# Optimization experiments

Measured on AMD Instinct MI355X. Metric: run time of the kernel, lower is better.

Reference implementation:

```python
import jax, jax.numpy as jnp
import numpy as np

ALPHA = 1.702
LIMIT = 7.0
EPS = 1e-5
TOP_K = 4


def setup_inputs() -> dict:
    key = jax.random.key(0)
    ks = jax.random.split(key, 8)
    B, S, H, I, E = 2, 512, 2048, 2048, 16
    return {
        "x": jax.random.normal(ks[0], (B, S, H), jnp.float32),
        "norm_w": jnp.ones((H,), jnp.float32),
        "gate_w": jax.random.normal(ks[1], (E, H), jnp.float32) * 0.02,
        "gate_b": jax.random.normal(ks[2], (E,), jnp.float32) * 0.02,
        "w1": jax.random.normal(ks[3], (E, 2 * I, H), jnp.float32) * 0.02,
        "b1": jax.random.normal(ks[4], (E, 2 * I), jnp.float32) * 0.02,
        "w2": jax.random.normal(ks[5], (E, H, I), jnp.float32) * 0.02,
        "b2": jax.random.normal(ks[6], (E, H), jnp.float32) * 0.02,
    }


def reference(x, norm_w, gate_w, gate_b, w1, b1, w2, b2):
    B, S, H = x.shape
    M = B * S
    E = gate_w.shape[0]
    xf = x.reshape(M, H)
    # RMSNorm
    t = xf * jax.lax.rsqrt(jnp.mean(xf * xf, axis=-1, keepdims=True) + EPS) * norm_w
    # Router: top-k over logits, then softmax over the selected k (sm_first=False)
    logits = t @ gate_w.T + gate_b  # [M, E]
    vals, idx = jax.lax.top_k(logits, TOP_K)
    gates_k = jax.nn.softmax(vals, axis=-1)  # [M, k]
    # Scatter top-k gate weights into dense [M, E] combine matrix
    G = jnp.zeros((M, E), x.dtype).at[jnp.arange(M)[:, None], idx].set(gates_k)
    # Expert MLP1 (all experts, combined sparsely below): [E, M, 2I]
    h = jnp.einsum('mh,eoh->emo', t, w1) + b1[:, None, :]
    # SwiGLU with clamp (gpt-oss): interleaved gate/linear columns
    a = jnp.minimum(h[..., ::2], LIMIT)
    b = jnp.clip(h[..., 1::2], -LIMIT, LIMIT)
    act = a * jax.nn.sigmoid(ALPHA * a) * (b + 1.0)  # [E, M, I]
    # Expert MLP2: [E, M, H]
    y = jnp.einsum('emi,edi->emd', act, w2) + b2[:, None, :]
    # Combine with gate weights (gammas scale full per-expert output incl. bias)
    delta = jnp.einsum('me,emd->md', G, y)
    return x + delta.reshape(B, S, H)
```

## Files before the change

kernel.cpp:

```cpp
#include <hip/hip_runtime.h>
#include <hip/hip_bf16.h>

constexpr int MTOK = 1024;
constexpr int HDIM = 2048;
constexpr int IDIM = 2048;
constexpr int NEXP = 16;
constexpr int TOPK = 4;
constexpr int NA   = MTOK * TOPK;

#define ALPHA_C 1.702f
#define LIMIT_C 7.0f
#define RMS_EPS 1e-5f

using short8 = __attribute__((ext_vector_type(8))) short;
using f32x4  = __attribute__((ext_vector_type(4))) float;

__device__ __forceinline__ unsigned short f2bf(float f) {
    unsigned u = __builtin_bit_cast(unsigned, f);
    u += 0x7fffu + ((u >> 16) & 1u);
    return (unsigned short)(u >> 16);
}

__device__ __forceinline__ unsigned pack2bf(float lo, float hi) {
    return (unsigned)f2bf(lo) | ((unsigned)f2bf(hi) << 16);
}

__device__ __forceinline__ short8 cvt8(const float4 a, const float4 b) {
    union { short8 s; unsigned u[4]; } r;
    r.u[0] = pack2bf(a.x, a.y);
    r.u[1] = pack2bf(a.z, a.w);
    r.u[2] = pack2bf(b.x, b.y);
    r.u[3] = pack2bf(b.z, b.w);
    return r.s;
}

__global__ __launch_bounds__(256) void k_router(
    const float* __restrict__ x, const float* __restrict__ norm_w,
    const float* __restrict__ gate_w, const float* __restrict__ gate_b,
    unsigned short* __restrict__ t_bf,
    int* __restrict__ counts, int* __restrict__ idx_of,
    int* __restrict__ slot_of, float* __restrict__ gate_mk)
{
    __shared__ float t_lds[HDIM];
    __shared__ float red[4];
    __shared__ float logits[NEXP];

    const int m   = blockIdx.x;
    const int tid = threadIdx.x;
    const float* xr = x + (size_t)m * HDIM;

    float4 v0 = ((const float4*)xr)[tid * 2];
    float4 v1 = ((const float4*)xr)[tid * 2 + 1];
    float ss = v0.x*v0.x + v0.y*v0.y + v0.z*v0.z + v0.w*v0.w
             + v1.x*v1.x + v1.y*v1.y + v1.z*v1.z + v1.w*v1.w;
    #pragma unroll
    for (int off = 32; off > 0; off >>= 1) ss += __shfl_down(ss, off);
    if ((tid & 63) == 0) red[tid >> 6] = ss;
    __syncthreads();
    float tot = red[0] + red[1] + red[2] + red[3];
    float scale = rsqrtf(tot / (float)HDIM + RMS_EPS);

    float4 n0 = ((const float4*)norm_w)[tid * 2];
    float4 n1 = ((const float4*)norm_w)[tid * 2 + 1];
    float t[8];
    t[0]=v0.x*scale*n0.x; t[1]=v0.y*scale*n0.y; t[2]=v0.z*scale*n0.z; t[3]=v0.w*scale*n0.w;
    t[4]=v1.x*scale*n1.x; t[5]=v1.y*scale*n1.y; t[6]=v1.z*scale*n1.z; t[7]=v1.w*scale*n1.w;
    short8 pk;
    #pragma unroll
    for (int j = 0; j < 8; ++j) {
        t_lds[tid * 8 + j] = t[j];
        pk[j] = (short)f2bf(t[j]);
    }
    *(short8*)(t_bf + (size_t)m * HDIM + tid * 8) = pk;
    __syncthreads();

    const int e = tid >> 4, j = tid & 15;
    const float4* gw4 = (const float4*)(gate_w + (size_t)e * HDIM);
    const float4* tl4 = (const float4*)t_lds;
    float part = 0.f;
    for (int h4 = j; h4 < HDIM / 4; h4 += 16) {
        float4 g = gw4[h4], tv = tl4[h4];
        part += g.x*tv.x + g.y*tv.y + g.z*tv.z + g.w*tv.w;
    }
    #pragma unroll
    for (int off = 8; off > 0; off >>= 1) part += __shfl_xor(part, off);
    if (j == 0) logits[e] = part + gate_b[e];
    __syncthreads();

    if (tid == 0) {
        float lv[NEXP];
        #pragma unroll
        for (int q = 0; q < NEXP; ++q) lv[q] = logits[q];
        int   sel[TOPK];
        float sv[TOPK];
        #pragma unroll
        for (int k = 0; k < TOPK; ++k) {
            float best = -1e30f; int bi = 0;
            for (int q = 0; q < NEXP; ++q)
                if (lv[q] > best) { best = lv[q]; bi = q; }
            sel[k] = bi; sv[k] = best; lv[bi] = -1e30f;
        }
        float mx = sv[0], s = 0.f, g[TOPK];
        #pragma unroll
        for (int k = 0; k < TOPK; ++k) { g[k] = __expf(sv[k] - mx); s += g[k]; }
        float inv = 1.f / s;
        #pragma unroll
        for (int k = 0; k < TOPK; ++k) {
            int a = m * TOPK + k;
            int slot = atomicAdd(&counts[sel[k]], 1);
            idx_of[a]  = sel[k];
            slot_of[a] = slot;
            gate_mk[a] = g[k] * inv;
        }
    }
}

__global__ void k_remap(const int* __restrict__ idx_of, const int* __restrict__ slot_of,
                        const int* __restrict__ counts,
                        int* __restrict__ token_of, int* __restrict__ rowidx)
{
    int a = blockIdx.x * blockDim.x + threadIdx.x;
    if (a >= NA) return;
    int e = idx_of[a];
    int off = 0;
    for (int q = 0; q < NEXP; ++q) off += (q < e) ? counts[q] : 0;
    int r = off + slot_of[a];
    token_of[r] = a >> 2;
    rowidx[a]   = r;
}

__global__ __launch_bounds__(256, 2) void k_gemm1(
    const unsigned short* __restrict__ t_bf,
    const float* __restrict__ w1, const float* __restrict__ b1,
    const int* __restrict__ counts, const int* __restrict__ token_of,
    unsigned short* __restrict__ act)
{
    __shared__ unsigned char lB[2][5120];

    const int e = blockIdx.z;
    int ne = 0, roff = 0;
    #pragma unroll
    for (int q = 0; q < NEXP; ++q) {
        int cq = counts[q];
        roff += (q < e) ? cq : 0;
        ne    = (q == e) ? cq : ne;
    }
    const int brow = blockIdx.y * 320;
    if (brow >= ne) return;
    const int i0 = blockIdx.x * 32;
    const int tid = threadIdx.x;

    const int wv = tid >> 6, ln = tid & 63;
    const int lr = ln & 15, lk = ln >> 4;
    const int br = tid >> 2, bp = tid & 3;

    const unsigned short* aptr[5];
    #pragma unroll
    for (int mf = 0; mf < 5; ++mf) {
        int rg = brow + wv * 80 + mf * 16 + lr;
        int tok = token_of[roff + (rg < ne ? rg : 0)];
        aptr[mf] = t_bf + (size_t)tok * HDIM + lk * 8;
    }
    const int o = (br < 32) ? (2 * (i0 + br)) : (2 * (i0 + br - 32) + 1);
    const float* bsrc = w1 + ((size_t)e * (2 * IDIM) + o) * HDIM + bp * 8;

    short8 aE[5], aO[5];
    float4 bS0[2], bS1[2], bS2[2], bS3[2];
    f32x4  acc[5][4] = {};

    constexpr int NT = 64;

    #pragma unroll
    for (int mf = 0; mf < 5; ++mf) aE[mf] = *(const short8*)(aptr[mf]);
    {
        float4 p0 = *(const float4*)(bsrc);
        float4 p1 = *(const float4*)(bsrc + 4);
        *(short8*)(&lB[0][br * 80 + bp * 16]) = cvt8(p0, p1);
    }
    bS1[0] = *(const float4*)(bsrc + 32);  bS1[1] = *(const float4*)(bsrc + 36);
    bS2[0] = *(const float4*)(bsrc + 64);  bS2[1] = *(const float4*)(bsrc + 68);
    asm volatile("s_waitcnt lgkmcnt(0)" ::: "memory");
    __builtin_amdgcn_s_barrier();

#define GSTEP(T_, AU, AP, SPUB, SISS)                                                    \
    {                                                                                    \
        const int t_ = (T_);                                                             \
        if (t_ + 1 < NT) {                                          \
            _Pragma("unroll")                                                            \
            for (int mf = 0; mf < 5; ++mf)                                               \
                AP[mf] = *(const short8*)(aptr[mf] + (t_ + 1) * 32);                     \
        }                                                                                \
        if (t_ + 3 < NT) {                                         \
            SISS[0] = *(const float4*)(bsrc + (t_ + 3) * 32);                            \
            SISS[1] = *(const float4*)(bsrc + (t_ + 3) * 32 + 4);                        \
        }                                                                                \
        __builtin_amdgcn_sched_barrier(0);                      \
        if (t_ + 1 < NT)                                          \
            *(short8*)(&lB[(t_ + 1) & 1][br * 80 + bp * 16]) = cvt8(SPUB[0], SPUB[1]);   \
        short8 bfr[4];                                            \
        _Pragma("unroll")                                                                \
        for (int n = 0; n < 4; ++n)                                                      \
            bfr[n] = *(const short8*)(&lB[t_ & 1][(n * 16 + lr) * 80 + lk * 16]);        \
        _Pragma("unroll")                                                                \
        for (int mf = 0; mf < 5; ++mf)                                                   \
            _Pragma("unroll")                                                            \
            for (int n = 0; n < 4; ++n)                                                  \
                acc[mf][n] = __builtin_amdgcn_mfma_f32_16x16x32_bf16(                    \
                    AU[mf], bfr[n], acc[mf][n], 0, 0, 0);                                \
        asm volatile("s_waitcnt lgkmcnt(0)" ::: "memory");                               \
        __builtin_amdgcn_s_barrier();                                                    \
    }

    for (int t4 = 0; t4 < NT / 4; ++t4) {
        const int tb = t4 * 4;
        GSTEP(tb + 0, aE, aO, bS1, bS3)
        GSTEP(tb + 1, aO, aE, bS2, bS0)
        GSTEP(tb + 2, aE, aO, bS3, bS1)
        GSTEP(tb + 3, aO, aE, bS0, bS2)
    }
#undef GSTEP

    #pragma unroll
    for (int n = 0; n < 2; ++n) {
        const int i = i0 + n * 16 + lr;
        const float ba = b1[(size_t)e * (2 * IDIM) + 2 * i];
        const float bb = b1[(size_t)e * (2 * IDIM) + 2 * i + 1];
        #pragma unroll
        for (int mf = 0; mf < 5; ++mf) {
            #pragma unroll
            for (int r = 0; r < 4; ++r) {
                const int rg = brow + wv * 80 + mf * 16 + lk * 4 + r;
                if (rg < ne) {
                    float ha = acc[mf][n][r] + ba;
                    float hb = acc[mf][n + 2][r] + bb;
                    float a = fminf(ha, LIMIT_C);
                    float b = fminf(fmaxf(hb, -LIMIT_C), LIMIT_C);
                    float s = 1.f / (1.f + __expf(-ALPHA_C * a));
                    act[(size_t)(roff + rg) * IDIM + i] = f2bf(a * s * (b + 1.f));
                }
            }
        }
    }
}

__global__ __launch_bounds__(256, 2) void k_gemm2(
    const unsigned short* __restrict__ act,
    const float* __restrict__ w2, const float* __restrict__ b2,
    const int* __restrict__ counts, const int* __restrict__ token_of,
    unsigned short* __restrict__ ybuf)
{
    __shared__ unsigned char lB[2][5120];

    const int e = blockIdx.z;
    int ne = 0, roff = 0;
    #pragma unroll
    for (int q = 0; q < NEXP; ++q) {
        int cq = counts[q];
        roff += (q < e) ? cq : 0;
        ne    = (q == e) ? cq : ne;
    }
    const int brow = blockIdx.y * 320;
    if (brow >= ne) return;
    const int d0 = blockIdx.x * 64;
    const int tid = threadIdx.x;

    const int wv = tid >> 6, ln = tid & 63;
    const int lr = ln & 15, lk = ln >> 4;
    const int br = tid >> 2, bp = tid & 3;

    const unsigned short* aptr[5];
    #pragma unroll
    for (int mf = 0; mf < 5; ++mf) {
        int rg = brow + wv * 80 + mf * 16 + lr;
        int rc = (rg < ne) ? rg : 0;
        aptr[mf] = act + (size_t)(roff + rc) * IDIM + lk * 8;
    }
    const float* bsrc = w2 + ((size_t)e * HDIM + d0 + br) * IDIM + bp * 8;

    short8 aE[5], aO[5];
    float4 bS0[2], bS1[2], bS2[2], bS3[2];
    f32x4  acc[5][4] = {};

    constexpr int NT = 64;

    #pragma unroll
    for (int mf = 0; mf < 5; ++mf) aE[mf] = *(const short8*)(aptr[mf]);
    {
        float4 p0 = *(const float4*)(bsrc);
        float4 p1 = *(const float4*)(bsrc + 4);
        *(short8*)(&lB[0][br * 80 + bp * 16]) = cvt8(p0, p1);
    }
    bS1[0] = *(const float4*)(bsrc + 32);  bS1[1] = *(const float4*)(bsrc + 36);
    bS2[0] = *(const float4*)(bsrc + 64);  bS2[1] = *(const float4*)(bsrc + 68);
    asm volatile("s_waitcnt lgkmcnt(0)" ::: "memory");
    __builtin_amdgcn_s_barrier();

#define GSTEP(T_, AU, AP, SPUB, SISS)                                                    \
    {                                                                                    \
        const int t_ = (T_);                                                             \
        if (t_ + 1 < NT) {                                                               \
            _Pragma("unroll")                                                            \
            for (int mf = 0; mf < 5; ++mf)                                               \
                AP[mf] = *(const short8*)(aptr[mf] + (t_ + 1) * 32);                     \
        }                                                                                \
        if (t_ + 3 < NT) {                                                               \
            SISS[0] = *(const float4*)(bsrc + (t_ + 3) * 32);                            \
            SISS[1] = *(const float4*)(bsrc + (t_ + 3) * 32 + 4);                        \
        }                                                                                \
        __builtin_amdgcn_sched_barrier(0);                                               \
        if (t_ + 1 < NT)                                                                 \
            *(short8*)(&lB[(t_ + 1) & 1][br * 80 + bp * 16]) = cvt8(SPUB[0], SPUB[1]);   \
        short8 bfr[4];                                                                   \
        _Pragma("unroll")                                                                \
        for (int n = 0; n < 4; ++n)                                                      \
            bfr[n] = *(const short8*)(&lB[t_ & 1][(n * 16 + lr) * 80 + lk * 16]);        \
        _Pragma("unroll")                                                                \
        for (int mf = 0; mf < 5; ++mf)                                                   \
            _Pragma("unroll")                                                            \
            for (int n = 0; n < 4; ++n)                                                  \
                acc[mf][n] = __builtin_amdgcn_mfma_f32_16x16x32_bf16(                    \
                    AU[mf], bfr[n], acc[mf][n], 0, 0, 0);                                \
        asm volatile("s_waitcnt lgkmcnt(0)" ::: "memory");                               \
        __builtin_amdgcn_s_barrier();                                                    \
    }

    for (int t4 = 0; t4 < NT / 4; ++t4) {
        const int tb = t4 * 4;
        GSTEP(tb + 0, aE, aO, bS1, bS3)
        GSTEP(tb + 1, aO, aE, bS2, bS0)
        GSTEP(tb + 2, aE, aO, bS3, bS1)
        GSTEP(tb + 3, aO, aE, bS0, bS2)
    }
#undef GSTEP

    #pragma unroll
    for (int mf = 0; mf < 5; ++mf) {
        #pragma unroll
        for (int r = 0; r < 4; ++r) {
            const int rg = brow + wv * 80 + mf * 16 + lk * 4 + r;
            if (rg >= ne) continue;
            unsigned short* yrow = ybuf + (size_t)(roff + rg) * HDIM;
            #pragma unroll
            for (int n = 0; n < 4; ++n) {
                const int d = d0 + n * 16 + lr;
                yrow[d] = f2bf(acc[mf][n][r] + b2[(size_t)e * HDIM + d]);
            }
        }
    }
}

__global__ __launch_bounds__(256) void k_comb(
    const float* __restrict__ x, const unsigned short* __restrict__ ybuf,
    const int* __restrict__ rowidx, const float* __restrict__ gate_mk,
    float* __restrict__ out)
{
    __shared__ int   rws[TOPK];
    __shared__ float gws[TOPK];
    const int m = blockIdx.x;
    const int tid = threadIdx.x;
    if (tid < TOPK) {
        rws[tid] = rowidx[m * TOPK + tid];
        gws[tid] = gate_mk[m * TOPK + tid];
    }
    __syncthreads();
    const int d = tid * 8;
    float4 o0 = ((const float4*)(x + (size_t)m * HDIM + d))[0];
    float4 o1 = ((const float4*)(x + (size_t)m * HDIM + d))[1];
    #pragma unroll
    for (int k = 0; k < TOPK; ++k) {
        const float g = gws[k];
        short8 y = *(const short8*)(ybuf + (size_t)rws[k] * HDIM + d);
        float yv[8];
        #pragma unroll
        for (int j = 0; j < 8; ++j) {
            unsigned u = ((unsigned)(unsigned short)y[j]) << 16;
            yv[j] = __builtin_bit_cast(float, u);
        }
        o0.x += g * yv[0]; o0.y += g * yv[1]; o0.z += g * yv[2]; o0.w += g * yv[3];
        o1.x += g * yv[4]; o1.y += g * yv[5]; o1.z += g * yv[6]; o1.w += g * yv[7];
    }
    ((float4*)(out + (size_t)m * HDIM + d))[0] = o0;
    ((float4*)(out + (size_t)m * HDIM + d))[1] = o1;
}

extern "C" void kernel_launch(void* const* d_in, const int* in_sizes, int n_in,
                              void* d_out, int out_size, void* d_ws, size_t ws_size,
                              hipStream_t stream) {
    const float* x      = (const float*)d_in[0];
    const float* norm_w = (const float*)d_in[1];
    const float* gate_w = (const float*)d_in[2];
    const float* gate_b = (const float*)d_in[3];
    const float* w1     = (const float*)d_in[4];
    const float* b1     = (const float*)d_in[5];
    const float* w2     = (const float*)d_in[6];
    const float* b2     = (const float*)d_in[7];
    float* out = (float*)d_out;

    char* ws = (char*)d_ws;
    size_t off = 0;
    unsigned short* t_bf = (unsigned short*)(ws + off); off += (size_t)MTOK * HDIM * 2;
    unsigned short* actb = (unsigned short*)(ws + off); off += (size_t)NA * IDIM * 2;
    unsigned short* ybuf = (unsigned short*)(ws + off); off += (size_t)NA * HDIM * 2;
    int*   counts   = (int*)(ws + off);   off += 256;
    int*   idx_of   = (int*)(ws + off);   off += (size_t)NA * 4;
    int*   slot_of  = (int*)(ws + off);   off += (size_t)NA * 4;
    float* gate_mk  = (float*)(ws + off); off += (size_t)NA * 4;
    int*   token_of = (int*)(ws + off);   off += (size_t)NA * 4;
    int*   rowidx   = (int*)(ws + off);   off += (size_t)NA * 4;

    (void)hipMemsetAsync(counts, 0, 256, stream);
    k_router<<<MTOK, 256, 0, stream>>>(x, norm_w, gate_w, gate_b, t_bf,
                                       counts, idx_of, slot_of, gate_mk);
    k_remap<<<NA / 256, 256, 0, stream>>>(idx_of, slot_of, counts,
                                          token_of, rowidx);
    k_gemm1<<<dim3(IDIM / 32, (MTOK + 319) / 320, NEXP), 256, 0, stream>>>(
        t_bf, w1, b1, counts, token_of, actb);
    k_gemm2<<<dim3(HDIM / 64, (MTOK + 319) / 320, NEXP), 256, 0, stream>>>(
        actb, w2, b2, counts, token_of, ybuf);
    k_comb<<<MTOK, 256, 0, stream>>>(x, ybuf, rowidx, gate_mk, out);
}
```

Measured before the change: 410.9 us.

## Restructure expert GEMMs with wider tiles, direct-to-LDS fp32 weight loads, XCD-aware block mapping

Both expert GEMMs now use 512-thread blocks with 8 waves arranged 4x2, covering 320 rows by 256 weight columns per block instead of 320x64. Weight tiles are copied as fp32 straight into a triple-buffered LDS ring with global_load_lds, and converted to bf16 with v_cvt_pk_bf16_f32 when read for the MFMA. Blocks use a flat 1D grid decoded so that each XCD handles two experts, aiming to improve L2 reuse of weights. The goal is fewer register-staged global loads and more MFMA work per weight byte, at the cost of 96KB of LDS per block and reconverting each weight element once per wave that reads it.

```diff
diff --git a/kernel.cpp b/kernel.cpp
--- a/kernel.cpp
+++ b/kernel.cpp
@@ -21,17 +21,16 @@
     return (unsigned short)(u >> 16);
 }
 
-__device__ __forceinline__ unsigned pack2bf(float lo, float hi) {
-    return (unsigned)f2bf(lo) | ((unsigned)f2bf(hi) << 16);
-}
-
-__device__ __forceinline__ short8 cvt8(const float4 a, const float4 b) {
-    union { short8 s; unsigned u[4]; } r;
-    r.u[0] = pack2bf(a.x, a.y);
-    r.u[1] = pack2bf(a.z, a.w);
-    r.u[2] = pack2bf(b.x, b.y);
-    r.u[3] = pack2bf(b.z, b.w);
-    return r.s;
+__device__ __forceinline__ void gload16(const void* g, void* l) {
+    __builtin_amdgcn_global_load_lds(
+        (const __attribute__((address_space(1))) void*)g,
+        (__attribute__((address_space(3))) void*)l, 16, 0, 0);
+}
+
+__device__ __forceinline__ unsigned cvtpk(float lo, float hi) {
+    unsigned r;
+    asm volatile("v_cvt_pk_bf16_f32 %0, %1, %2" : "=v"(r) : "v"(lo), "v"(hi));
+    return r;
 }
 
 __global__ __launch_bounds__(256) void k_router(
@@ -129,15 +128,59 @@
     rowidx[a]   = r;
 }
 
-__global__ __launch_bounds__(256, 2) void k_gemm1(
+
+#define GEMM_STEP(T_, RB, WB, AU, AP, NTT)                                               \
+    {                                                                                    \
+        const int t_ = (T_);                                                             \
+        __builtin_amdgcn_s_barrier();                                                    \
+        const int tw = (t_ + 2 < (NTT)) ? (t_ + 2) : ((NTT) - 1);                        \
+        _Pragma("unroll")                                                                \
+        for (int j = 0; j < 4; ++j)                                                      \
+            gload16(bsrc + (size_t)j * BJSTR + (size_t)tw * 32,                          \
+                    lds + (WB) * 32768 + (wv * 4 + j) * 1024);                           \
+        const int ta = (t_ + 1 < (NTT)) ? (t_ + 1) : ((NTT) - 1);                        \
+        _Pragma("unroll")                                                                \
+        for (int mf = 0; mf < 5; ++mf)                                                   \
+            AP[mf] = *(const short8*)(aptr[mf] + ta * 32);                               \
+        asm volatile("s_waitcnt vmcnt(9)" ::: "memory");                                 \
+        __builtin_amdgcn_sched_barrier(0);                                               \
+        short8 bfr[8];                                                                   \
+        _Pragma("unroll")                                                                \
+        for (int n = 0; n < 8; ++n) {                                                    \
+            const int c_ = cfrag[n] + lr;                                                \
+            const unsigned char* cb = lds + (RB) * 32768 + (c_ >> 3) * 1024              \
+                                      + (c_ & 7) * 16 + lk * 256;                        \
+            f32x4 u0 = *(const f32x4*)(cb);                                              \
+            f32x4 u1 = *(const f32x4*)(cb + 128);                                        \
+            union { short8 s; unsigned u[4]; } r;                                        \
+            r.u[0] = cvtpk(u0[0], u0[1]); r.u[1] = cvtpk(u0[2], u0[3]);                  \
+            r.u[2] = cvtpk(u1[0], u1[1]); r.u[3] = cvtpk(u1[2], u1[3]);                  \
+            bfr[n] = r.s;                                                                \
+        }                                                                                \
+        _Pragma("unroll")                                                                \
+        for (int mf = 0; mf < 5; ++mf)                                                   \
+            _Pragma("unroll")                                                            \
+            for (int n = 0; n < 8; ++n)                                                  \
+                acc[mf][n] = __builtin_amdgcn_mfma_f32_16x16x32_bf16(                    \
+                    AU[mf], bfr[n], acc[mf][n], 0, 0, 0);                                \
+    }
+
+__global__ __launch_bounds__(512, 2) void k_gemm1(
     const unsigned short* __restrict__ t_bf,
     const float* __restrict__ w1, const float* __restrict__ b1,
     const int* __restrict__ counts, const int* __restrict__ token_of,
     unsigned short* __restrict__ act)
 {
-    __shared__ unsigned char lB[2][5120];
-
-    const int e = blockIdx.z;
+    __shared__ unsigned char lB[3 * 32768];
+
+    const int bid = blockIdx.x;
+    const int xcd = bid & 7;
+    const int jj  = bid >> 3;
+    const int e   = (xcd << 1) | (jj & 1);
+    const int rem = jj >> 1;
+    const int by  = rem >> 4;
+    const int bx  = rem & 15;
+
     int ne = 0, roff = 0;
     #pragma unroll
     for (int q = 0; q < NEXP; ++q) {
@@ -145,94 +188,75 @@
         roff += (q < e) ? cq : 0;
         ne    = (q == e) ? cq : ne;
     }
-    const int brow = blockIdx.y * 320;
+    const int brow = by * 320;
     if (brow >= ne) return;
-    const int i0 = blockIdx.x * 32;
+    const int i0 = bx * 128;
     const int tid = threadIdx.x;
 
     const int wv = tid >> 6, ln = tid & 63;
+    const int wm = wv >> 1, wn = wv & 1;
     const int lr = ln & 15, lk = ln >> 4;
-    const int br = tid >> 2, bp = tid & 3;
+
+    unsigned char* lds = lB;
+    constexpr int NT = 64;
 
     const unsigned short* aptr[5];
     #pragma unroll
     for (int mf = 0; mf < 5; ++mf) {
-        int rg = brow + wv * 80 + mf * 16 + lr;
+        int rg = brow + wm * 80 + mf * 16 + lr;
         int tok = token_of[roff + (rg < ne ? rg : 0)];
         aptr[mf] = t_bf + (size_t)tok * HDIM + lk * 8;
     }
-    const int o = (br < 32) ? (2 * (i0 + br)) : (2 * (i0 + br - 32) + 1);
-    const float* bsrc = w1 + ((size_t)e * (2 * IDIM) + o) * HDIM + bp * 8;
+
+    const int c7 = ln & 7, chunk = ln >> 3;
+    const int col0 = wv * 32 + c7;
+    const int o0 = (col0 < 128) ? (2 * (i0 + col0)) : (2 * (i0 + col0 - 128) + 1);
+    const float* bsrc = w1 + ((size_t)e * (2 * IDIM) + o0) * HDIM + chunk * 4;
+    const size_t BJSTR = (size_t)16 * HDIM;
+
+    int cfrag[8];
+    #pragma unroll
+    for (int n = 0; n < 4; ++n) { cfrag[n] = wn * 64 + n * 16; cfrag[n + 4] = 128 + wn * 64 + n * 16; }
 
     short8 aE[5], aO[5];
-    float4 bS0[2], bS1[2], bS2[2], bS3[2];
-    f32x4  acc[5][4] = {};
-
-    constexpr int NT = 64;
-
+    f32x4  acc[5][8] = {};
+
+    #pragma unroll
+    for (int j = 0; j < 4; ++j)
+        gload16(bsrc + (size_t)j * BJSTR, lds + (wv * 4 + j) * 1024);
     #pragma unroll
     for (int mf = 0; mf < 5; ++mf) aE[mf] = *(const short8*)(aptr[mf]);
-    {
-        float4 p0 = *(const float4*)(bsrc);
-        float4 p1 = *(const float4*)(bsrc + 4);
-        *(short8*)(&lB[0][br * 80 + bp * 16]) = cvt8(p0, p1);
-    }
-    bS1[0] = *(const float4*)(bsrc + 32);  bS1[1] = *(const float4*)(bsrc + 36);
-    bS2[0] = *(const float4*)(bsrc + 64);  bS2[1] = *(const float4*)(bsrc + 68);
-    asm volatile("s_waitcnt lgkmcnt(0)" ::: "memory");
-    __builtin_amdgcn_s_barrier();
-
-#define GSTEP(T_, AU, AP, SPUB, SISS)                                                    \
-    {                                                                                    \
-        const int t_ = (T_);                                                             \
-        if (t_ + 1 < NT) {                                          \
-            _Pragma("unroll")                                                            \
-            for (int mf = 0; mf < 5; ++mf)                                               \
-                AP[mf] = *(const short8*)(aptr[mf] + (t_ + 1) * 32);                     \
-        }                                                                                \
-        if (t_ + 3 < NT) {                                         \
-            SISS[0] = *(const float4*)(bsrc + (t_ + 3) * 32);                            \
-            SISS[1] = *(const float4*)(bsrc + (t_ + 3) * 32 + 4);                        \
-        }                                                                                \
-        __builtin_amdgcn_sched_barrier(0);                      \
-        if (t_ + 1 < NT)                                          \
-            *(short8*)(&lB[(t_ + 1) & 1][br * 80 + bp * 16]) = cvt8(SPUB[0], SPUB[1]);   \
-        short8 bfr[4];                                            \
-        _Pragma("unroll")                                                                \
-        for (int n = 0; n < 4; ++n)                                                      \
-            bfr[n] = *(const short8*)(&lB[t_ & 1][(n * 16 + lr) * 80 + lk * 16]);        \
-        _Pragma("unroll")                                                                \
-        for (int mf = 0; mf < 5; ++mf)                                                   \
-            _Pragma("unroll")                                                            \
-            for (int n = 0; n < 4; ++n)                                                  \
-                acc[mf][n] = __builtin_amdgcn_mfma_f32_16x16x32_bf16(                    \
-                    AU[mf], bfr[n], acc[mf][n], 0, 0, 0);                                \
-        asm volatile("s_waitcnt lgkmcnt(0)" ::: "memory");                               \
-        __builtin_amdgcn_s_barrier();                                                    \
-    }
-
-    for (int t4 = 0; t4 < NT / 4; ++t4) {
-        const int tb = t4 * 4;
-        GSTEP(tb + 0, aE, aO, bS1, bS3)
-        GSTEP(tb + 1, aO, aE, bS2, bS0)
-        GSTEP(tb + 2, aE, aO, bS3, bS1)
-        GSTEP(tb + 3, aO, aE, bS0, bS2)
-    }
-#undef GSTEP
-
-    #pragma unroll
-    for (int n = 0; n < 2; ++n) {
-        const int i = i0 + n * 16 + lr;
+    #pragma unroll
+    for (int j = 0; j < 4; ++j)
+        gload16(bsrc + (size_t)j * BJSTR + 32, lds + 32768 + (wv * 4 + j) * 1024);
+
+    for (int q = 0; q < 10; ++q) {
+        const int tb = q * 6;
+        GEMM_STEP(tb + 0, 0, 2, aE, aO, NT)
+        GEMM_STEP(tb + 1, 1, 0, aO, aE, NT)
+        GEMM_STEP(tb + 2, 2, 1, aE, aO, NT)
+        GEMM_STEP(tb + 3, 0, 2, aO, aE, NT)
+        GEMM_STEP(tb + 4, 1, 0, aE, aO, NT)
+        GEMM_STEP(tb + 5, 2, 1, aO, aE, NT)
+    }
+    GEMM_STEP(60, 0, 2, aE, aO, NT)
+    GEMM_STEP(61, 1, 0, aO, aE, NT)
+    GEMM_STEP(62, 2, 1, aE, aO, NT)
+    GEMM_STEP(63, 0, 2, aO, aE, NT)
+
+    #pragma unroll
+    for (int n = 0; n < 4; ++n) {
+        const int i = i0 + wn * 64 + n * 16 + lr;
         const float ba = b1[(size_t)e * (2 * IDIM) + 2 * i];
         const float bb = b1[(size_t)e * (2 * IDIM) + 2 * i + 1];
         #pragma unroll
         for (int mf = 0; mf < 5; ++mf) {
             #pragma unroll
             for (int r = 0; r < 4; ++r) {
-                const int rg = brow + wv * 80 + mf * 16 + lk * 4 + r;
+                const int rg = brow + wm * 80 + mf * 16 + lk * 4 + r;
                 if (rg < ne) {
                     float ha = acc[mf][n][r] + ba;
-                    float hb = acc[mf][n + 2][r] + bb;
+                    float hb = acc[mf][n + 4][r] + bb;
                     float a = fminf(ha, LIMIT_C);
                     float b = fminf(fmaxf(hb, -LIMIT_C), LIMIT_C);
                     float s = 1.f / (1.f + __expf(-ALPHA_C * a));
@@ -243,15 +267,22 @@
     }
 }
 
-__global__ __launch_bounds__(256, 2) void k_gemm2(
+__global__ __launch_bounds__(512, 2) void k_gemm2(
     const unsigned short* __restrict__ act,
     const float* __restrict__ w2, const float* __restrict__ b2,
     const int* __restrict__ counts, const int* __restrict__ token_of,
     unsigned short* __restrict__ ybuf)
 {
-    __shared__ unsigned char lB[2][5120];
-
-    const int e = blockIdx.z;
+    __shared__ unsigned char lB[3 * 32768];
+
+    const int bid = blockIdx.x;
+    const int xcd = bid & 7;
+    const int jj  = bid >> 3;
+    const int e   = (xcd << 1) | (jj & 1);
+    const int rem = jj >> 1;
+    const int by  = rem >> 3;
+    const int bx  = rem & 7;
+
     int ne = 0, roff = 0;
     #pragma unroll
     for (int q = 0; q < NEXP; ++q) {
@@ -259,90 +290,71 @@
         roff += (q < e) ? cq : 0;
         ne    = (q == e) ? cq : ne;
     }
-    const int brow = blockIdx.y * 320;
+    const int brow = by * 320;
     if (brow >= ne) return;
-    const int d0 = blockIdx.x * 64;
+    const int d0 = bx * 256;
     const int tid = threadIdx.x;
 
     const int wv = tid >> 6, ln = tid & 63;
+    const int wm = wv >> 1, wn = wv & 1;
     const int lr = ln & 15, lk = ln >> 4;
-    const int br = tid >> 2, bp = tid & 3;
+
+    unsigned char* lds = lB;
+    constexpr int NT = 64;
 
     const unsigned short* aptr[5];
     #pragma unroll
     for (int mf = 0; mf < 5; ++mf) {
-        int rg = brow + wv * 80 + mf * 16 + lr;
+        int rg = brow + wm * 80 + mf * 16 + lr;
         int rc = (rg < ne) ? rg : 0;
         aptr[mf] = act + (size_t)(roff + rc) * IDIM + lk * 8;
     }
-    const float* bsrc = w2 + ((size_t)e * HDIM + d0 + br) * IDIM + bp * 8;
+
+    const int c7 = ln & 7, chunk = ln >> 3;
+    const int col0 = wv * 32 + c7;
+    const float* bsrc = w2 + ((size_t)e * HDIM + d0 + col0) * IDIM + chunk * 4;
+    const size_t BJSTR = (size_t)8 * IDIM;
+
+    int cfrag[8];
+    #pragma unroll
+    for (int n = 0; n < 8; ++n) cfrag[n] = wn * 128 + n * 16;
 
     short8 aE[5], aO[5];
-    float4 bS0[2], bS1[2], bS2[2], bS3[2];
-    f32x4  acc[5][4] = {};
-
-    constexpr int NT = 64;
-
+    f32x4  acc[5][8] = {};
+
+    #pragma unroll
+    for (int j = 0; j < 4; ++j)
+        gload16(bsrc + (size_t)j * BJSTR, lds + (wv * 4 + j) * 1024);
     #pragma unroll
     for (int mf = 0; mf < 5; ++mf) aE[mf] = *(const short8*)(aptr[mf]);
-    {
-        float4 p0 = *(const float4*)(bsrc);
-        float4 p1 = *(const float4*)(bsrc + 4);
-        *(short8*)(&lB[0][br * 80 + bp * 16]) = cvt8(p0, p1);
-    }
-    bS1[0] = *(const float4*)(bsrc + 32);  bS1[1] = *(const float4*)(bsrc + 36);
-    bS2[0] = *(const float4*)(bsrc + 64);  bS2[1] = *(const float4*)(bsrc + 68);
-    asm volatile("s_waitcnt lgkmcnt(0)" ::: "memory");
-    __builtin_amdgcn_s_barrier();
-
-#define GSTEP(T_, AU, AP, SPUB, SISS)                                                    \
-    {                                                                                    \
-        const int t_ = (T_);                                                             \
-        if (t_ + 1 < NT) {                                                               \
-            _Pragma("unroll")                                                            \
-            for (int mf = 0; mf < 5; ++mf)                                               \
-                AP[mf] = *(const short8*)(aptr[mf] + (t_ + 1) * 32);                     \
-        }                                                                                \
-        if (t_ + 3 < NT) {                                                               \
-            SISS[0] = *(const float4*)(bsrc + (t_ + 3) * 32);                            \
-            SISS[1] = *(const float4*)(bsrc + (t_ + 3) * 32 + 4);                        \
-        }                                                                                \
-        __builtin_amdgcn_sched_barrier(0);                                               \
-        if (t_ + 1 < NT)                                                                 \
-            *(short8*)(&lB[(t_ + 1) & 1][br * 80 + bp * 16]) = cvt8(SPUB[0], SPUB[1]);   \
-        short8 bfr[4];                                                                   \
-        _Pragma("unroll")                                                                \
-        for (int n = 0; n < 4; ++n)                                                      \
-            bfr[n] = *(const short8*)(&lB[t_ & 1][(n * 16 + lr) * 80 + lk * 16]);        \
-        _Pragma("unroll")                                                                \
-        for (int mf = 0; mf < 5; ++mf)                                                   \
-            _Pragma("unroll")                                                            \
-            for (int n = 0; n < 4; ++n)                                                  \
-                acc[mf][n] = __builtin_amdgcn_mfma_f32_16x16x32_bf16(                    \
-                    AU[mf], bfr[n], acc[mf][n], 0, 0, 0);                                \
-        asm volatile("s_waitcnt lgkmcnt(0)" ::: "memory");                               \
-        __builtin_amdgcn_s_barrier();                                                    \
-    }
-
-    for (int t4 = 0; t4 < NT / 4; ++t4) {
-        const int tb = t4 * 4;
-        GSTEP(tb + 0, aE, aO, bS1, bS3)
-        GSTEP(tb + 1, aO, aE, bS2, bS0)
-        GSTEP(tb + 2, aE, aO, bS3, bS1)
-        GSTEP(tb + 3, aO, aE, bS0, bS2)
-    }
-#undef GSTEP
+    #pragma unroll
+    for (int j = 0; j < 4; ++j)
+        gload16(bsrc + (size_t)j * BJSTR + 32, lds + 32768 + (wv * 4 + j) * 1024);
+
+    for (int q = 0; q < 10; ++q) {
+        const int tb = q * 6;
+        GEMM_STEP(tb + 0, 0, 2, aE, aO, NT)
+        GEMM_STEP(tb + 1, 1, 0, aO, aE, NT)
+        GEMM_STEP(tb + 2, 2, 1, aE, aO, NT)
+        GEMM_STEP(tb + 3, 0, 2, aO, aE, NT)
+        GEMM_STEP(tb + 4, 1, 0, aE, aO, NT)
+        GEMM_STEP(tb + 5, 2, 1, aO, aE, NT)
+    }
+    GEMM_STEP(60, 0, 2, aE, aO, NT)
+    GEMM_STEP(61, 1, 0, aO, aE, NT)
+    GEMM_STEP(62, 2, 1, aE, aO, NT)
+    GEMM_STEP(63, 0, 2, aO, aE, NT)
 
     #pragma unroll
     for (int mf = 0; mf < 5; ++mf) {
         #pragma unroll
         for (int r = 0; r < 4; ++r) {
-            const int rg = brow + wv * 80 + mf * 16 + lk * 4 + r;
+            const int rg = brow + wm * 80 + mf * 16 + lk * 4 + r;
             if (rg >= ne) continue;
             unsigned short* yrow = ybuf + (size_t)(roff + rg) * HDIM;
             #pragma unroll
-            for (int n = 0; n < 4; ++n) {
-                const int d = d0 + n * 16 + lr;
+            for (int n = 0; n < 8; ++n) {
+                const int d = d0 + cfrag[n] + lr;
                 yrow[d] = f2bf(acc[mf][n][r] + b2[(size_t)e * HDIM + d]);
             }
         }
@@ -413,9 +425,7 @@
                                        counts, idx_of, slot_of, gate_mk);
     k_remap<<<NA / 256, 256, 0, stream>>>(idx_of, slot_of, counts,
                                           token_of, rowidx);
-    k_gemm1<<<dim3(IDIM / 32, (MTOK + 319) / 320, NEXP), 256, 0, stream>>>(
-        t_bf, w1, b1, counts, token_of, actb);
-    k_gemm2<<<dim3(HDIM / 64, (MTOK + 319) / 320, NEXP), 256, 0, stream>>>(
-        actb, w2, b2, counts, token_of, ybuf);
+    k_gemm1<<<8 * 2 * 4 * 16, 512, 0, stream>>>(t_bf, w1, b1, counts, token_of, actb);
+    k_gemm2<<<8 * 2 * 4 * 8, 512, 0, stream>>>(actb, w2, b2, counts, token_of, ybuf);
     k_comb<<<MTOK, 256, 0, stream>>>(x, ybuf, rowidx, gate_mk, out);
 }
```

After: 967.7 us. 136% more time.
